# Performance work log

Hardware: AMD Instinct MI355X
Metric: run time of the kernel (lower is better)

Reference implementation:

```python
import jax, jax.numpy as jnp
import numpy as np

EPSILON = 1e-6
CANVAS_H, CANVAS_W = 256, 256
NUM_SAMPLES = 64  # num curve samples; also num arc-length approximation segments
BATCH = 16
NUM_KEY_POINTS = 4  # cubic Bezier control points


def eval_bezier(ctrl, ts):
    """De Casteljau evaluation. ctrl: [K,2], ts: [T] -> [T,2]. Grad-safe at t=0,1."""
    K = ctrl.shape[0]
    def one(t):
        pts = ctrl
        for _ in range(K - 1):
            pts = (1.0 - t) * pts[:-1] + t * pts[1:]
        return pts[0]
    return jax.vmap(one)(ts)


def sample_points_one(ctrl):
    """Arc-length-uniform samples along the Bezier curve (BezierCurve with
    num_approximations linear segments + get_uniform_ts). ctrl: [K,2] -> [S,2]."""
    ts0 = jnp.linspace(0.0, 1.0, NUM_SAMPLES)
    pts0 = eval_bezier(ctrl, ts0)                                   # [S,2]
    seg = jnp.linalg.norm(jnp.diff(pts0, axis=0), axis=1)           # [S-1]
    cum = jnp.concatenate([jnp.zeros((1,), pts0.dtype), jnp.cumsum(seg)])
    u = cum / (cum[-1] + EPSILON)                                   # normalized arc length
    t_arc = jnp.interp(ts0, u, ts0)                                 # arc-length -> param t
    return eval_bezier(ctrl, t_arc)


def setup_inputs() -> dict:
    key = jax.random.key(0)
    k1, k2, k3 = jax.random.split(key, 3)
    inputs = jax.random.uniform(k1, (BATCH, NUM_KEY_POINTS, 2), dtype=jnp.float32)
    # widths in pixels (positive, realistic stroke widths); aa exponents > 1
    widths = jax.random.uniform(k2, (BATCH,), dtype=jnp.float32) * 8.0 + 2.0
    aa_factors = jax.random.uniform(k3, (BATCH,), dtype=jnp.float32) * 3.0 + 1.0
    return {"inputs": inputs, "widths": widths, "aa_factors": aa_factors}


def reference(inputs, widths, aa_factors):
    canvas_shape = jnp.asarray([CANVAS_H, CANVAS_W], dtype=inputs.dtype)
    key_points = inputs * canvas_shape[None, None, :]               # [B,K,2] in (y,x)
    sample_points = jax.vmap(sample_points_one)(key_points)         # [B,S,2]

    # pixel center positions in (y, x) order, row-major over the canvas
    ys, xs = jnp.meshgrid(jnp.arange(CANVAS_H), jnp.arange(CANVAS_W), indexing="ij")
    positions = jnp.stack([ys, xs], axis=-1).reshape(-1, 2).astype(inputs.dtype)  # [P,2]

    # dense pairwise distances [B,S,P] then min over samples -> [B,P]
    diff = sample_points[:, :, None, :] - positions[None, None, :, :]
    distances = jnp.linalg.norm(diff, axis=-1)
    minimum_distances = jnp.min(distances, axis=1)                  # [B,P]

    canvas = minimum_distances / widths[:, None]
    canvas = (canvas + EPSILON) ** aa_factors[:, None]
    canvas = jnp.clip(1.0 - canvas, 0.0, 1.0)
    return canvas.reshape(inputs.shape[0], CANVAS_H, CANVAS_W)
```

## Files before the change

### kernel.cpp

```cpp
#include <hip/hip_runtime.h>


#define EPSILON 1e-6f
#define NS 64

__device__ __forceinline__ void bezier4(const float cy[4], const float cx[4],
                                        float t, float& ry, float& rx) {
    float s = 1.0f - t;
    float ay0 = s * cy[0] + t * cy[1];
    float ay1 = s * cy[1] + t * cy[2];
    float ay2 = s * cy[2] + t * cy[3];
    float by0 = s * ay0 + t * ay1;
    float by1 = s * ay1 + t * ay2;
    ry = s * by0 + t * by1;
    float ax0 = s * cx[0] + t * cx[1];
    float ax1 = s * cx[1] + t * cx[2];
    float ax2 = s * cx[2] + t * cx[3];
    float bx0 = s * ax0 + t * ax1;
    float bx1 = s * ax1 + t * ax2;
    rx = s * bx0 + t * bx1;
}

__global__ __launch_bounds__(256) void curve_kernel(
    const float* __restrict__ inputs,
    const float* __restrict__ widths,
    const float* __restrict__ aas,
    float* __restrict__ out)
{
    __shared__ float s_y0[NS], s_x0[NS];
    __shared__ float s_seg[NS];
    __shared__ float s_cum[NS];
    __shared__ float s_total;
    __shared__ float2 s_pts[NS];

    const int b       = blockIdx.x >> 6;
    const int rowbase = (blockIdx.x & 63) << 2;
    const int tid     = threadIdx.x;

    float cy[4], cx[4];
    if (tid < NS) {
        #pragma unroll
        for (int i = 0; i < 4; ++i) {
            cy[i] = inputs[b * 8 + 2 * i + 0] * 256.0f;
            cx[i] = inputs[b * 8 + 2 * i + 1] * 256.0f;
        }
        const float t0 = (float)tid / 63.0f;
        float py, px;
        bezier4(cy, cx, t0, py, px);
        s_y0[tid] = py;
        s_x0[tid] = px;
    }
    __syncthreads();

    if (tid < NS - 1) {
        float dy = s_y0[tid + 1] - s_y0[tid];
        float dx = s_x0[tid + 1] - s_x0[tid];
        s_seg[tid] = sqrtf(dy * dy + dx * dx);
    }
    __syncthreads();

    if (tid == 0) {
        float c = 0.0f;
        s_cum[0] = 0.0f;
        #pragma unroll
        for (int l = 1; l < NS; ++l) {
            c += s_seg[l - 1];
            s_cum[l] = c;
        }
        s_total = c;
    }
    __syncthreads();

    if (tid < NS) {
        const float t0   = (float)tid / 63.0f;
        const float invT = 1.0f / (s_total + EPSILON);
        int lo = 0, hi = 63;
        #pragma unroll
        for (int it = 0; it < 6; ++it) {
            int mid = (lo + hi + 1) >> 1;
            if (s_cum[mid] * invT <= t0) lo = mid; else hi = mid - 1;
        }
        float t_arc;
        if (lo >= 63) {
            t_arc = 1.0f;
        } else {
            float uj    = s_cum[lo] * invT;
            float uj1   = s_cum[lo + 1] * invT;
            float denom = uj1 - uj;
            float tsj   = (float)lo / 63.0f;
            t_arc = (denom > 0.0f)
                  ? tsj + (t0 - uj) / denom * (1.0f / 63.0f)
                  : tsj;
        }
        float sy, sx;
        bezier4(cy, cx, t_arc, sy, sx);
        s_pts[tid] = make_float2(sy, sx);
    }
    __syncthreads();

    const float w    = widths[b];
    const float aa   = aas[b];
    const float invw = 1.0f / w;

    const int wave = tid >> 6;
    const int lane = tid & 63;
    const int row  = rowbase + wave;
    const float pyf = (float)row;
    const float px0 = (float)(lane << 2);

    float m0 = 1e30f, m1 = 1e30f, m2 = 1e30f, m3 = 1e30f;
    #pragma unroll 8
    for (int i = 0; i < NS; ++i) {
        float2 sp = s_pts[i];
        float dy  = sp.x - pyf;
        float dy2 = dy * dy;
        float dx  = sp.y - px0;
        float d0 = fmaf(dx, dx, dy2); m0 = fminf(m0, d0); dx -= 1.0f;
        float d1 = fmaf(dx, dx, dy2); m1 = fminf(m1, d1); dx -= 1.0f;
        float d2 = fmaf(dx, dx, dy2); m2 = fminf(m2, d2); dx -= 1.0f;
        float d3 = fmaf(dx, dx, dy2); m3 = fminf(m3, d3);
    }

    float ms[4] = { m0, m1, m2, m3 };
    float vv[4];
    #pragma unroll
    for (int k = 0; k < 4; ++k) {
        float md = sqrtf(ms[k]);
        float c  = md * invw + EPSILON;
        float v  = 1.0f - exp2f(aa * log2f(c));
        vv[k] = fminf(fmaxf(v, 0.0f), 1.0f);
    }

    const int base = (b << 16) | (row << 8) | (lane << 2);
    reinterpret_cast<float4*>(out)[base >> 2] =
        make_float4(vv[0], vv[1], vv[2], vv[3]);
}

extern "C" void kernel_launch(void* const* d_in, const int* in_sizes, int n_in,
                              void* d_out, int out_size, void* d_ws, size_t ws_size,
                              hipStream_t stream) {
    const float* inp = (const float*)d_in[0];
    const float* wid = (const float*)d_in[1];
    const float* aaf = (const float*)d_in[2];
    float* out = (float*)d_out;

    dim3 grid(16 * 64);
    dim3 block(256);
    hipLaunchKernelGGL(curve_kernel, grid, block, 0, stream,
                       inp, wid, aaf, out);
}
```

Measured before the change: 64.02 us.

## Compute 8 pixels per thread, halve grid, and simplify curve preprocessing

```diff
diff --git a/kernel.cpp b/kernel.cpp
--- a/kernel.cpp
+++ b/kernel.cpp
@@ -27,14 +27,13 @@
     const float* __restrict__ aas,
     float* __restrict__ out)
 {
-    __shared__ float s_y0[NS], s_x0[NS];
     __shared__ float s_seg[NS];
     __shared__ float s_cum[NS];
     __shared__ float s_total;
     __shared__ float2 s_pts[NS];
 
-    const int b       = blockIdx.x >> 6;
-    const int rowbase = (blockIdx.x & 63) << 2;
+    const int b       = blockIdx.x >> 5;
+    const int rowbase = (blockIdx.x & 31) << 3;
     const int tid     = threadIdx.x;
 
     float cy[4], cx[4];
@@ -44,18 +43,13 @@
             cy[i] = inputs[b * 8 + 2 * i + 0] * 256.0f;
             cx[i] = inputs[b * 8 + 2 * i + 1] * 256.0f;
         }
-        const float t0 = (float)tid / 63.0f;
-        float py, px;
-        bezier4(cy, cx, t0, py, px);
-        s_y0[tid] = py;
-        s_x0[tid] = px;
-    }
-    __syncthreads();
-
-    if (tid < NS - 1) {
-        float dy = s_y0[tid + 1] - s_y0[tid];
-        float dx = s_x0[tid + 1] - s_x0[tid];
-        s_seg[tid] = sqrtf(dy * dy + dx * dx);
+        if (tid < NS - 1) {
+            float py, px, qy, qx;
+            bezier4(cy, cx, (float)tid / 63.0f, py, px);
+            bezier4(cy, cx, (float)(tid + 1) / 63.0f, qy, qx);
+            float dy = qy - py, dx = qx - px;
+            s_seg[tid] = sqrtf(dy * dy + dx * dx);
+        }
     }
     __syncthreads();
 
@@ -74,12 +68,11 @@
     if (tid < NS) {
         const float t0   = (float)tid / 63.0f;
         const float invT = 1.0f / (s_total + EPSILON);
-        int lo = 0, hi = 63;
+        int cnt = 0;
         #pragma unroll
-        for (int it = 0; it < 6; ++it) {
-            int mid = (lo + hi + 1) >> 1;
-            if (s_cum[mid] * invT <= t0) lo = mid; else hi = mid - 1;
-        }
+        for (int j = 0; j < NS; ++j)
+            cnt += (s_cum[j] * invT <= t0) ? 1 : 0;
+        int lo = cnt - 1;
         float t_arc;
         if (lo >= 63) {
             t_arc = 1.0f;
@@ -104,36 +97,41 @@
 
     const int wave = tid >> 6;
     const int lane = tid & 63;
-    const int row  = rowbase + wave;
+    const int row  = rowbase + (wave << 1) + (lane >> 5);
     const float pyf = (float)row;
-    const float px0 = (float)(lane << 2);
+    const float px0 = (float)((lane & 31) << 3);
 
-    float m0 = 1e30f, m1 = 1e30f, m2 = 1e30f, m3 = 1e30f;
+    float m[8];
+    #pragma unroll
+    for (int k = 0; k < 8; ++k) m[k] = 1e30f;
+
     #pragma unroll 8
     for (int i = 0; i < NS; ++i) {
         float2 sp = s_pts[i];
         float dy  = sp.x - pyf;
         float dy2 = dy * dy;
         float dx  = sp.y - px0;
-        float d0 = fmaf(dx, dx, dy2); m0 = fminf(m0, d0); dx -= 1.0f;
-        float d1 = fmaf(dx, dx, dy2); m1 = fminf(m1, d1); dx -= 1.0f;
-        float d2 = fmaf(dx, dx, dy2); m2 = fminf(m2, d2); dx -= 1.0f;
-        float d3 = fmaf(dx, dx, dy2); m3 = fminf(m3, d3);
+        #pragma unroll
+        for (int k = 0; k < 8; ++k) {
+            float d = fmaf(dx, dx, dy2);
+            m[k] = fminf(m[k], d);
+            dx -= 1.0f;
+        }
     }
 
-    float ms[4] = { m0, m1, m2, m3 };
-    float vv[4];
+    float vv[8];
     #pragma unroll
-    for (int k = 0; k < 4; ++k) {
-        float md = sqrtf(ms[k]);
+    for (int k = 0; k < 8; ++k) {
+        float md = sqrtf(m[k]);
         float c  = md * invw + EPSILON;
         float v  = 1.0f - exp2f(aa * log2f(c));
         vv[k] = fminf(fmaxf(v, 0.0f), 1.0f);
     }
 
-    const int base = (b << 16) | (row << 8) | (lane << 2);
-    reinterpret_cast<float4*>(out)[base >> 2] =
-        make_float4(vv[0], vv[1], vv[2], vv[3]);
+    const int base = (b << 16) | (row << 8) | ((lane & 31) << 3);
+    float4* o4 = reinterpret_cast<float4*>(out);
+    o4[(base >> 2) + 0] = make_float4(vv[0], vv[1], vv[2], vv[3]);
+    o4[(base >> 2) + 1] = make_float4(vv[4], vv[5], vv[6], vv[7]);
 }
 
 extern "C" void kernel_launch(void* const* d_in, const int* in_sizes, int n_in,
@@ -144,7 +142,7 @@
     const float* aaf = (const float*)d_in[2];
     float* out = (float*)d_out;
 
-    dim3 grid(16 * 64);
+    dim3 grid(16 * 32);
     dim3 block(256);
     hipLaunchKernelGGL(curve_kernel, grid, block, 0, stream,
                        inp, wid, aaf, out);
```

New measurement: 64.67 us. No clear change (+1.0%).
